# Optimization experiments

Measured on AMD Instinct MI355X. Metric: run time of the kernel, lower is better.

## Reference

```python
import jax, jax.numpy as jnp
import numpy as np


def setup_inputs() -> dict:
    key = jax.random.key(0)
    ks = jax.random.split(key, 8)
    bs, G, A, C, CM, D, H = 256, 169, 3, 5, 32, 1024, 512
    return {
        "boxes_sml0": jax.random.uniform(ks[0], (bs, G, A, C), dtype=jnp.float32),
        "masks_in0": jax.random.normal(ks[1], (bs, G, A, CM), dtype=jnp.float32),
        "feat": jax.random.normal(ks[2], (bs, D, 13, 13), dtype=jnp.float32),
        "lang_feat": jax.random.normal(ks[3], (bs, H), dtype=jnp.float32),
        "W_vs": jax.random.normal(ks[4], (D, H), dtype=jnp.float32) * 0.02,
        "b_vs": jnp.zeros((H,), dtype=jnp.float32),
        "W_ts": jax.random.normal(ks[5], (H, H), dtype=jnp.float32) * 0.02,
        "b_ts": jnp.zeros((H,), dtype=jnp.float32),
        "select_num": 32,
    }


def reference(boxes_sml0, masks_in0, feat, lang_feat, W_vs, b_vs, W_ts, b_ts, select_num):
    bs, G, A, C = boxes_sml0.shape
    CM = masks_in0.shape[-1]
    D = feat.shape[1]

    # mean over anchors of objectness channel 4 -> top-k grid selection
    mean_score = jnp.mean(boxes_sml0[..., 4], axis=2)           # [bs, G]
    _, idx = jax.lax.top_k(mean_score, select_num)              # [bs, k]

    # scatter-mask + masked_select in torch == gather of selected grids
    boxes_new = jnp.take_along_axis(boxes_sml0, idx[:, :, None, None], axis=1)  # [bs,k,A,C]
    masks_new = jnp.take_along_axis(masks_in0, idx[:, :, None, None], axis=1)   # [bs,k,A,CM]

    # gather visual features of selected grids, project
    i_all = feat.reshape(bs, D, -1).transpose(0, 2, 1)          # [bs, G, D]
    i_sel = jnp.take_along_axis(i_all, idx[:, :, None], axis=1) # [bs, k, D]
    x_new = i_sel @ W_vs + b_vs                                 # [bs, k, H]
    y_new = lang_feat @ W_ts + b_ts                             # [bs, H]

    # head: visual-text similarity, pick top grid per batch
    sim = jnp.einsum('bkh,bh->bk', x_new, y_new)                # [bs, k]
    maxval = jnp.max(sim, axis=1)                               # [bs]
    pred = jnp.argmax(sim, axis=1)                              # [bs]

    sel_b = jnp.take_along_axis(boxes_new, pred[:, None, None, None], axis=1)[:, 0]  # [bs,A,C]
    sel_m = jnp.take_along_axis(masks_new, pred[:, None, None, None], axis=1)[:, 0]  # [bs,A,CM]

    # cxcywh -> xyxy with original in-place overwrite semantics
    cx, cy, w, h = sel_b[..., 0], sel_b[..., 1], sel_b[..., 2], sel_b[..., 3]
    x1 = cx - w / 2
    y1 = cy - h / 2
    x2 = x1 + w
    y2 = y1 + h
    refined = jnp.concatenate(
        [jnp.stack([x1, y1, x2, y2], axis=-1), sel_b[..., 4:]], axis=-1)  # [bs,A,C]

    # pick anchor with max objectness, gather 5-dim box and mask coeffs
    aidx = jnp.argmax(refined[..., 4], axis=1)                  # [bs]
    box_new = jnp.take_along_axis(refined[..., :5], aidx[:, None, None], axis=1)  # [bs,1,5]
    mask_new = jnp.take_along_axis(sel_m, aidx[:, None, None], axis=1)            # [bs,1,CM]
    return box_new, mask_new, maxval
```

## Files before the change

### kernel.cpp

```cpp
#include <hip/hip_runtime.h>
#include <cfloat>
#include <cstdint>

#define GBM 64
#define GBN 64
#define GBK 64
#define GPAD 68

#define G_    169
#define D_    1024
#define SLAB  256
#define ROWG  8
#define NGRP  32
#define GRPF  1352
#define NV    338
#define SPL   8

typedef unsigned int u32;

__device__ __forceinline__ void gload_lds16(const float* g, float* l) {
    __builtin_amdgcn_global_load_lds(
        (const __attribute__((address_space(1))) u32*)g,
        (__attribute__((address_space(3))) u32*)l, 16, 0, 0);
}

__device__ __forceinline__ void stage_group(const float* gsrc, float* ldsbase, int lane) {
    #pragma unroll
    for (int j = 0; j < 6; j++) {
        int idx = j * 64 + lane;
        if (idx < NV)
            gload_lds16(gsrc + 4 * idx, ldsbase + j * 256);
    }
}

__global__ __launch_bounds__(256) void gemm_splitk(
    const float* __restrict__ A, const float* __restrict__ B,
    float* __restrict__ Cpart, int M, int N, int K)
{
    __shared__ __align__(16) float Asm[GBK][GPAD];
    __shared__ __align__(16) float Bsm[GBK][GPAD];
    int t  = threadIdx.x;
    int m0 = blockIdx.y * GBM, n0 = blockIdx.x * GBN;
    int ks = blockIdx.z * GBK;

    #pragma unroll
    for (int i = 0; i < 4; i++) {
        int v = t + 256 * i;
        int m = v >> 4, k4 = (v & 15) * 4;
        float4 x = *(const float4*)&A[(size_t)(m0 + m) * K + ks + k4];
        Asm[k4 + 0][m] = x.x; Asm[k4 + 1][m] = x.y;
        Asm[k4 + 2][m] = x.z; Asm[k4 + 3][m] = x.w;
    }
    #pragma unroll
    for (int i = 0; i < 4; i++) {
        int v = t + 256 * i;
        int r = v >> 4, c4 = (v & 15) * 4;
        *(float4*)&Bsm[r][c4] = *(const float4*)&B[(size_t)(ks + r) * N + n0 + c4];
    }
    __syncthreads();

    int r4 = (t >> 4) * 4, c4 = (t & 15) * 4;
    float acc[4][4] = {{0.f}};
    #pragma unroll
    for (int kk = 0; kk < GBK; kk++) {
        float4 a = *(const float4*)&Asm[kk][r4];
        float4 b = *(const float4*)&Bsm[kk][c4];
        float av[4] = {a.x, a.y, a.z, a.w};
        float bv[4] = {b.x, b.y, b.z, b.w};
        #pragma unroll
        for (int i = 0; i < 4; i++)
            #pragma unroll
            for (int j = 0; j < 4; j++) acc[i][j] += av[i] * bv[j];
    }
    float* Cp = Cpart + (size_t)blockIdx.z * M * N;
    #pragma unroll
    for (int i = 0; i < 4; i++) {
        float4 v = {acc[i][0], acc[i][1], acc[i][2], acc[i][3]};
        *(float4*)&Cp[(size_t)(m0 + r4 + i) * N + n0 + c4] = v;
    }
}

__global__ __launch_bounds__(256) void gemm2_fused(
    const float* __restrict__ py, const float* __restrict__ b_ts,
    const float* __restrict__ W, float* __restrict__ pz,
    int M, int N, int K)
{
    __shared__ __align__(16) float Asm[GBK][GPAD];
    __shared__ __align__(16) float Bsm[GBK][GPAD];
    int t  = threadIdx.x;
    int m0 = blockIdx.y * GBM, n0 = blockIdx.x * GBN;
    int ks = blockIdx.z * GBK;

    #pragma unroll
    for (int i = 0; i < 4; i++) {
        int v = t + 256 * i;
        int m = v >> 4, h4 = (v & 15) * 4;
        float4 x = *(const float4*)&b_ts[ks + h4];
        #pragma unroll
        for (int s = 0; s < SPL; s++) {
            float4 p = *(const float4*)&py[((size_t)s * M + m0 + m) * K + ks + h4];
            x.x += p.x; x.y += p.y; x.z += p.z; x.w += p.w;
        }
        Asm[h4 + 0][m] = x.x; Asm[h4 + 1][m] = x.y;
        Asm[h4 + 2][m] = x.z; Asm[h4 + 3][m] = x.w;
    }
    #pragma unroll
    for (int i = 0; i < 4; i++) {
        int v = t + 256 * i;
        int n = v >> 4, k4 = (v & 15) * 4;
        float4 x = *(const float4*)&W[(size_t)(n0 + n) * K + ks + k4];
        Bsm[k4 + 0][n] = x.x; Bsm[k4 + 1][n] = x.y;
        Bsm[k4 + 2][n] = x.z; Bsm[k4 + 3][n] = x.w;
    }
    __syncthreads();

    int r4 = (t >> 4) * 4, c4 = (t & 15) * 4;
    float acc[4][4] = {{0.f}};
    #pragma unroll
    for (int kk = 0; kk < GBK; kk++) {
        float4 a = *(const float4*)&Asm[kk][r4];
        float4 b = *(const float4*)&Bsm[kk][c4];
        float av[4] = {a.x, a.y, a.z, a.w};
        float bv[4] = {b.x, b.y, b.z, b.w};
        #pragma unroll
        for (int i = 0; i < 4; i++)
            #pragma unroll
            for (int j = 0; j < 4; j++) acc[i][j] += av[i] * bv[j];
    }
    float* Cp = pz + (size_t)blockIdx.z * M * N;
    #pragma unroll
    for (int i = 0; i < 4; i++) {
        float4 v = {acc[i][0], acc[i][1], acc[i][2], acc[i][3]};
        *(float4*)&Cp[(size_t)(m0 + r4 + i) * N + n0 + c4] = v;
    }
}

__global__ __launch_bounds__(256) void feat_final(
    const float* __restrict__ feat, const float* __restrict__ pz,
    const float* __restrict__ boxes, const float* __restrict__ masks,
    const float* __restrict__ py, const float* __restrict__ b_ts,
    const float* __restrict__ b_vs, const int* __restrict__ kptr,
    float* __restrict__ out_box, float* __restrict__ out_mask,
    float* __restrict__ out_max,
    int bs, int AN, int CH, int CM, int H)
{
    __shared__ __align__(16) float buf[4][2][GRPF];
    __shared__ __align__(16) float zs[D_];
    __shared__ float accw[4 * 192];
    __shared__ float simall[176];
    __shared__ float ms[176];
    __shared__ int   selg[176];
    __shared__ float simv[176];
    __shared__ float redw[4];
    __shared__ float bbs;
    __shared__ int   selp[2];

    const int b = blockIdx.x;
    const int t = threadIdx.x;
    const int w = t >> 6, lane = t & 63;

    {
        int h4 = t * 4;
        float4 s = {0.f, 0.f, 0.f, 0.f};
        #pragma unroll
        for (int sp = 0; sp < SPL; sp++) {
            float4 v = *(const float4*)&pz[((size_t)sp * bs + b) * D_ + h4];
            s.x += v.x; s.y += v.y; s.z += v.z; s.w += v.w;
        }
        *(float4*)&zs[h4] = s;
    }

    const float* gsrc = feat + ((size_t)b * D_ + (size_t)w * SLAB) * G_;
    stage_group(gsrc, buf[w][0], lane);

    float acc0 = 0.f, acc1 = 0.f, acc2 = 0.f;
    const bool g2 = lane < (G_ - 128);
    int cur = 0;
    for (int gi = 0; gi < NGRP; gi++) {
        if (gi + 1 < NGRP) {
            stage_group(gsrc + (size_t)(gi + 1) * GRPF, buf[w][cur ^ 1], lane);
            asm volatile("s_waitcnt vmcnt(6)" ::: "memory");
        } else {
            asm volatile("s_waitcnt vmcnt(0)" ::: "memory");
        }
        __builtin_amdgcn_sched_barrier(0);
        const float* bp = buf[w][cur];
        const float* zp = &zs[w * SLAB + gi * ROWG];
        #pragma unroll
        for (int r = 0; r < ROWG; r++) {
            float zv = zp[r];
            acc0 += bp[r * G_ + lane] * zv;
            acc1 += bp[r * G_ + lane + 64] * zv;
            if (g2) acc2 += bp[r * G_ + lane + 128] * zv;
        }
        cur ^= 1;
    }
    accw[w * 192 + lane]       = acc0;
    accw[w * 192 + lane + 64]  = acc1;
    if (g2) accw[w * 192 + lane + 128] = acc2;
    __syncthreads();

    int k = *kptr; if (k > G_) k = G_;

    if (t < G_) {
        simall[t] = accw[t] + accw[192 + t] + accw[384 + t] + accw[576 + t];
        const float* bp = boxes + (size_t)(b * G_ + t) * AN * CH;
        float s = 0.f;
        for (int a = 0; a < AN; a++) s += bp[a * CH + 4];
        ms[t] = s / (float)AN;
    }
    float part = 0.f;
    for (int h = t; h < H; h += 256) {
        float yv = b_ts[h];
        #pragma unroll
        for (int s = 0; s < SPL; s++) yv += py[((size_t)s * bs + b) * H + h];
        part += b_vs[h] * yv;
    }
    #pragma unroll
    for (int off = 32; off > 0; off >>= 1) part += __shfl_down(part, off);
    if ((t & 63) == 0) redw[t >> 6] = part;
    __syncthreads();
    if (t == 0) bbs = redw[0] + redw[1] + redw[2] + redw[3];

    if (t < G_) {
        float mv = ms[t];
        int rank = 0;
        for (int g = 0; g < G_; g++) {
            float o = ms[g];
            rank += (int)((o > mv) | ((o == mv) & (g < t)));
        }
        if (rank < k) selg[rank] = t;
    }
    __syncthreads();

    if (t < k) simv[t] = simall[selg[t]];
    __syncthreads();

    if (t == 0) {
        float best = -FLT_MAX; int br = 0;
        for (int r = 0; r < k; r++) if (simv[r] > best) { best = simv[r]; br = r; }
        int gs = selg[br];
        const float* bp = boxes + (size_t)(b * G_ + gs) * AN * CH;
        float bo = -FLT_MAX; int ai = 0;
        for (int a = 0; a < AN; a++) { float o = bp[a * CH + 4]; if (o > bo) { bo = o; ai = a; } }
        float cx = bp[ai * CH + 0], cy = bp[ai * CH + 1];
        float ww = bp[ai * CH + 2], hh = bp[ai * CH + 3];
        float x1 = cx - ww * 0.5f, y1 = cy - hh * 0.5f;
        out_box[(size_t)b * CH + 0] = x1;
        out_box[(size_t)b * CH + 1] = y1;
        out_box[(size_t)b * CH + 2] = x1 + ww;
        out_box[(size_t)b * CH + 3] = y1 + hh;
        for (int c = 4; c < CH; c++) out_box[(size_t)b * CH + c] = bp[ai * CH + c];
        out_max[b] = best + bbs;
        selp[0] = gs; selp[1] = ai;
    }
    __syncthreads();
    if (t < CM) {
        out_mask[(size_t)b * CM + t] =
            masks[((size_t)(b * G_ + selp[0]) * AN + selp[1]) * CM + t];
    }
}

extern "C" void kernel_launch(void* const* d_in, const int* in_sizes, int n_in,
                              void* d_out, int out_size, void* d_ws, size_t ws_size,
                              hipStream_t stream)
{
    const float* boxes = (const float*)d_in[0];
    const float* masks = (const float*)d_in[1];
    const float* feat  = (const float*)d_in[2];
    const float* lang  = (const float*)d_in[3];
    const float* W_vs  = (const float*)d_in[4];
    const float* b_vs  = (const float*)d_in[5];
    const float* W_ts  = (const float*)d_in[6];
    const float* b_ts  = (const float*)d_in[7];
    const int*   kptr  = (const int*)d_in[8];

    int H  = in_sizes[5];
    int D  = in_sizes[4] / H;
    int bs = in_sizes[3] / H;
    int AN = 3;
    int CH = in_sizes[0] / (bs * G_ * AN);
    int CM = in_sizes[1] / (bs * G_ * AN);

    float* py = (float*)d_ws;
    float* pz = py + (size_t)SPL * bs * H;

    float* out_box  = (float*)d_out;
    float* out_mask = out_box + (size_t)bs * CH;
    float* out_max  = out_mask + (size_t)bs * CM;

    dim3 g1(H / GBN, bs / GBM, SPL);
    gemm_splitk<<<g1, 256, 0, stream>>>(lang, W_ts, py, bs, H, H);
    dim3 g2(D / GBN, bs / GBM, SPL);
    gemm2_fused<<<g2, 256, 0, stream>>>(py, b_ts, W_vs, pz, bs, D, H);
    feat_final<<<bs, 256, 0, stream>>>(feat, pz, boxes, masks, py, b_ts, b_vs,
                                       kptr, out_box, out_mask, out_max,
                                       bs, AN, CH, CM, H);
}
```

Before: 60.99 us.

## Use 8 waves and triple-buffered LDS staging in feat_final

Doubles the block to 512 threads (8 waves, each handling a 128-channel slab) and moves from double to triple buffering of the feature staging, with two groups in flight and adjusted vmcnt waits. The aim is more memory-level parallelism per CU for the bandwidth-bound feat reduction over the 1024x169 per-batch slab. It also adds a missing __syncthreads after filling zs, which the wider slab layout now requires. LDS use grows to about 8*3*1352 floats (~130KB), which may limit occupancy to one block per CU or exceed the LDS budget.

```diff
diff --git a/kernel.cpp b/kernel.cpp
--- a/kernel.cpp
+++ b/kernel.cpp
@@ -9,11 +9,13 @@
 
 #define G_    169
 #define D_    1024
-#define SLAB  256
+#define NW    8
+#define SLAB  128
 #define ROWG  8
-#define NGRP  32
+#define NGRP  16
 #define GRPF  1352
 #define NV    338
+#define NBUF  3
 #define SPL   8
 
 typedef unsigned int u32;
@@ -135,7 +137,7 @@
     }
 }
 
-__global__ __launch_bounds__(256) void feat_final(
+__global__ __launch_bounds__(512) void feat_final(
     const float* __restrict__ feat, const float* __restrict__ pz,
     const float* __restrict__ boxes, const float* __restrict__ masks,
     const float* __restrict__ py, const float* __restrict__ b_ts,
@@ -144,14 +146,14 @@
     float* __restrict__ out_max,
     int bs, int AN, int CH, int CM, int H)
 {
-    __shared__ __align__(16) float buf[4][2][GRPF];
+    __shared__ __align__(16) float buf[NW][NBUF][GRPF];
     __shared__ __align__(16) float zs[D_];
-    __shared__ float accw[4 * 192];
+    __shared__ float accw[NW * 192];
     __shared__ float simall[176];
     __shared__ float ms[176];
     __shared__ int   selg[176];
     __shared__ float simv[176];
-    __shared__ float redw[4];
+    __shared__ float redw[NW];
     __shared__ float bbs;
     __shared__ int   selp[2];
 
@@ -160,31 +162,34 @@
     const int w = t >> 6, lane = t & 63;
 
     {
-        int h4 = t * 4;
-        float4 s = {0.f, 0.f, 0.f, 0.f};
+        int h2 = t * 2;
+        float2 s = {0.f, 0.f};
         #pragma unroll
         for (int sp = 0; sp < SPL; sp++) {
-            float4 v = *(const float4*)&pz[((size_t)sp * bs + b) * D_ + h4];
-            s.x += v.x; s.y += v.y; s.z += v.z; s.w += v.w;
-        }
-        *(float4*)&zs[h4] = s;
-    }
+            float2 v = *(const float2*)&pz[((size_t)sp * bs + b) * D_ + h2];
+            s.x += v.x; s.y += v.y;
+        }
+        *(float2*)&zs[h2] = s;
+    }
+    __syncthreads();
 
     const float* gsrc = feat + ((size_t)b * D_ + (size_t)w * SLAB) * G_;
-    stage_group(gsrc, buf[w][0], lane);
+    stage_group(gsrc,        buf[w][0], lane);
+    stage_group(gsrc + GRPF, buf[w][1], lane);
 
     float acc0 = 0.f, acc1 = 0.f, acc2 = 0.f;
     const bool g2 = lane < (G_ - 128);
-    int cur = 0;
     for (int gi = 0; gi < NGRP; gi++) {
-        if (gi + 1 < NGRP) {
-            stage_group(gsrc + (size_t)(gi + 1) * GRPF, buf[w][cur ^ 1], lane);
+        if (gi + 2 < NGRP) {
+            stage_group(gsrc + (size_t)(gi + 2) * GRPF, buf[w][(gi + 2) % NBUF], lane);
+            asm volatile("s_waitcnt vmcnt(12)" ::: "memory");
+        } else if (gi + 1 < NGRP) {
             asm volatile("s_waitcnt vmcnt(6)" ::: "memory");
         } else {
             asm volatile("s_waitcnt vmcnt(0)" ::: "memory");
         }
         __builtin_amdgcn_sched_barrier(0);
-        const float* bp = buf[w][cur];
+        const float* bp = buf[w][gi % NBUF];
         const float* zp = &zs[w * SLAB + gi * ROWG];
         #pragma unroll
         for (int r = 0; r < ROWG; r++) {
@@ -193,7 +198,6 @@
             acc1 += bp[r * G_ + lane + 64] * zv;
             if (g2) acc2 += bp[r * G_ + lane + 128] * zv;
         }
-        cur ^= 1;
     }
     accw[w * 192 + lane]       = acc0;
     accw[w * 192 + lane + 64]  = acc1;
@@ -203,24 +207,34 @@
     int k = *kptr; if (k > G_) k = G_;
 
     if (t < G_) {
-        simall[t] = accw[t] + accw[192 + t] + accw[384 + t] + accw[576 + t];
+        float s = 0.f;
+        #pragma unroll
+        for (int ww = 0; ww < NW; ww++) s += accw[ww * 192 + t];
+        simall[t] = s;
         const float* bp = boxes + (size_t)(b * G_ + t) * AN * CH;
+        float o = 0.f;
+        for (int a = 0; a < AN; a++) o += bp[a * CH + 4];
+        ms[t] = o / (float)AN;
+    }
+    {
+        float part = 0.f;
+        for (int h = t; h < H; h += 512) {
+            float yv = b_ts[h];
+            #pragma unroll
+            for (int s = 0; s < SPL; s++) yv += py[((size_t)s * bs + b) * H + h];
+            part += b_vs[h] * yv;
+        }
+        #pragma unroll
+        for (int off = 32; off > 0; off >>= 1) part += __shfl_down(part, off);
+        if (lane == 0) redw[w] = part;
+    }
+    __syncthreads();
+    if (t == 0) {
         float s = 0.f;
-        for (int a = 0; a < AN; a++) s += bp[a * CH + 4];
-        ms[t] = s / (float)AN;
-    }
-    float part = 0.f;
-    for (int h = t; h < H; h += 256) {
-        float yv = b_ts[h];
-        #pragma unroll
-        for (int s = 0; s < SPL; s++) yv += py[((size_t)s * bs + b) * H + h];
-        part += b_vs[h] * yv;
-    }
-    #pragma unroll
-    for (int off = 32; off > 0; off >>= 1) part += __shfl_down(part, off);
-    if ((t & 63) == 0) redw[t >> 6] = part;
-    __syncthreads();
-    if (t == 0) bbs = redw[0] + redw[1] + redw[2] + redw[3];
+        #pragma unroll
+        for (int ww = 0; ww < NW; ww++) s += redw[ww];
+        bbs = s;
+    }
 
     if (t < G_) {
         float mv = ms[t];
@@ -293,7 +307,7 @@
     gemm_splitk<<<g1, 256, 0, stream>>>(lang, W_ts, py, bs, H, H);
     dim3 g2(D / GBN, bs / GBM, SPL);
     gemm2_fused<<<g2, 256, 0, stream>>>(py, b_ts, W_vs, pz, bs, D, H);
-    feat_final<<<bs, 256, 0, stream>>>(feat, pz, boxes, masks, py, b_ts, b_vs,
+    feat_final<<<bs, 512, 0, stream>>>(feat, pz, boxes, masks, py, b_ts, b_vs,
                                        kptr, out_box, out_mask, out_max,
                                        bs, AN, CH, CM, H);
 }
```

Result: faster. 57.68 us (-5.4%).

## Split feature dot-product across D into separate kernel with triple-buffered LDS staging

Applied to the files above, without the earlier changes.

The per-batch feature-dot kernel is split into a feat_dot kernel launched over an (8 D-slices × bs) grid and a separate finalize kernel. Each feat_dot block reduces a 128-channel slice with a three-stage global-to-LDS prefetch, reads z values by wave shuffle instead of an LDS copy, and writes partial similarity scores to workspace. finalize sums the 8 partials only for the selected top-k grids. This raises the block count from 256 to 2048 to hide the latency of the 177 MB feat read, at the cost of an extra launch and a partial-sum round trip through workspace.

```diff
diff --git a/kernel.cpp b/kernel.cpp
--- a/kernel.cpp
+++ b/kernel.cpp
@@ -9,11 +9,12 @@
 
 #define G_    169
 #define D_    1024
-#define SLAB  256
-#define ROWG  8
-#define NGRP  32
-#define GRPF  1352
-#define NV    338
+#define DSPLIT 8
+#define ROWG  4
+#define NGRP  8
+#define CHF   676
+#define CNV   169
+#define NBUF  3
 #define SPL   8
 
 typedef unsigned int u32;
@@ -24,12 +25,12 @@
         (__attribute__((address_space(3))) u32*)l, 16, 0, 0);
 }
 
-__device__ __forceinline__ void stage_group(const float* gsrc, float* ldsbase, int lane) {
-    #pragma unroll
-    for (int j = 0; j < 6; j++) {
+__device__ __forceinline__ void stage4(const float* g, float* l, int lane) {
+    #pragma unroll
+    for (int j = 0; j < 3; j++) {
         int idx = j * 64 + lane;
-        if (idx < NV)
-            gload_lds16(gsrc + 4 * idx, ldsbase + j * 256);
+        if (idx < CNV)
+            gload_lds16(g + 4 * idx, l + j * 256);
     }
 }
 
@@ -135,75 +136,78 @@
     }
 }
 
-__global__ __launch_bounds__(256) void feat_final(
+__global__ __launch_bounds__(256) void feat_dot(
     const float* __restrict__ feat, const float* __restrict__ pz,
+    float* __restrict__ s_part, int bs)
+{
+    __shared__ __align__(16) float buf[4][NBUF][CHF];
+    __shared__ float accw[4 * 176];
+    const int b = blockIdx.y, ds = blockIdx.x;
+    const int t = threadIdx.x, w = t >> 6, lane = t & 63;
+
+    float zreg = 0.f;
+    {
+        int zi = ds * 128 + w * 32 + (lane & 31);
+        #pragma unroll
+        for (int s = 0; s < SPL; s++)
+            zreg += pz[((size_t)s * bs + b) * D_ + zi];
+    }
+
+    const float* gsrc = feat + ((size_t)b * D_ + ds * 128 + w * 32) * G_;
+    stage4(gsrc,       buf[w][0], lane);
+    stage4(gsrc + CHF, buf[w][1], lane);
+
+    float acc0 = 0.f, acc1 = 0.f, acc2 = 0.f;
+    const bool g2 = lane < (G_ - 128);
+    for (int gi = 0; gi < NGRP; gi++) {
+        if (gi + 2 < NGRP) {
+            stage4(gsrc + (size_t)(gi + 2) * CHF, buf[w][(gi + 2) % NBUF], lane);
+            asm volatile("s_waitcnt vmcnt(6)" ::: "memory");
+        } else if (gi + 1 < NGRP) {
+            asm volatile("s_waitcnt vmcnt(3)" ::: "memory");
+        } else {
+            asm volatile("s_waitcnt vmcnt(0)" ::: "memory");
+        }
+        __builtin_amdgcn_sched_barrier(0);
+        const float* bp = buf[w][gi % NBUF];
+        #pragma unroll
+        for (int r = 0; r < ROWG; r++) {
+            float zv = __shfl(zreg, gi * 4 + r, 64);
+            acc0 += bp[r * G_ + lane] * zv;
+            acc1 += bp[r * G_ + lane + 64] * zv;
+            if (g2) acc2 += bp[r * G_ + lane + 128] * zv;
+        }
+    }
+    accw[w * 176 + lane]      = acc0;
+    accw[w * 176 + lane + 64] = acc1;
+    if (g2) accw[w * 176 + lane + 128] = acc2;
+    __syncthreads();
+    if (t < G_) {
+        float s = accw[t] + accw[176 + t] + accw[352 + t] + accw[528 + t];
+        s_part[((size_t)b * G_ + t) * DSPLIT + ds] = s;
+    }
+}
+
+__global__ __launch_bounds__(256) void finalize(
     const float* __restrict__ boxes, const float* __restrict__ masks,
-    const float* __restrict__ py, const float* __restrict__ b_ts,
-    const float* __restrict__ b_vs, const int* __restrict__ kptr,
+    const float* __restrict__ s_part, const float* __restrict__ py,
+    const float* __restrict__ b_ts, const float* __restrict__ b_vs,
+    const int* __restrict__ kptr,
     float* __restrict__ out_box, float* __restrict__ out_mask,
     float* __restrict__ out_max,
-    int bs, int AN, int CH, int CM, int H)
-{
-    __shared__ __align__(16) float buf[4][2][GRPF];
-    __shared__ __align__(16) float zs[D_];
-    __shared__ float accw[4 * 192];
-    __shared__ float simall[176];
+    int AN, int CH, int CM, int H, int bs)
+{
     __shared__ float ms[176];
     __shared__ int   selg[176];
     __shared__ float simv[176];
     __shared__ float redw[4];
-    __shared__ float bbs;
-    __shared__ int   selp[2];
-
-    const int b = blockIdx.x;
-    const int t = threadIdx.x;
-    const int w = t >> 6, lane = t & 63;
-
-    {
-        int h4 = t * 4;
-        float4 s = {0.f, 0.f, 0.f, 0.f};
-        #pragma unroll
-        for (int sp = 0; sp < SPL; sp++) {
-            float4 v = *(const float4*)&pz[((size_t)sp * bs + b) * D_ + h4];
-            s.x += v.x; s.y += v.y; s.z += v.z; s.w += v.w;
-        }
-        *(float4*)&zs[h4] = s;
-    }
-
-    const float* gsrc = feat + ((size_t)b * D_ + (size_t)w * SLAB) * G_;
-    stage_group(gsrc, buf[w][0], lane);
-
-    float acc0 = 0.f, acc1 = 0.f, acc2 = 0.f;
-    const bool g2 = lane < (G_ - 128);
-    int cur = 0;
-    for (int gi = 0; gi < NGRP; gi++) {
-        if (gi + 1 < NGRP) {
-            stage_group(gsrc + (size_t)(gi + 1) * GRPF, buf[w][cur ^ 1], lane);
-            asm volatile("s_waitcnt vmcnt(6)" ::: "memory");
-        } else {
-            asm volatile("s_waitcnt vmcnt(0)" ::: "memory");
-        }
-        __builtin_amdgcn_sched_barrier(0);
-        const float* bp = buf[w][cur];
-        const float* zp = &zs[w * SLAB + gi * ROWG];
-        #pragma unroll
-        for (int r = 0; r < ROWG; r++) {
-            float zv = zp[r];
-            acc0 += bp[r * G_ + lane] * zv;
-            acc1 += bp[r * G_ + lane + 64] * zv;
-            if (g2) acc2 += bp[r * G_ + lane + 128] * zv;
-        }
-        cur ^= 1;
-    }
-    accw[w * 192 + lane]       = acc0;
-    accw[w * 192 + lane + 64]  = acc1;
-    if (g2) accw[w * 192 + lane + 128] = acc2;
-    __syncthreads();
-
+    __shared__ float bb_s;
+    __shared__ int   sel_pair[2];
+
+    int b = blockIdx.x, t = threadIdx.x;
     int k = *kptr; if (k > G_) k = G_;
 
     if (t < G_) {
-        simall[t] = accw[t] + accw[192 + t] + accw[384 + t] + accw[576 + t];
         const float* bp = boxes + (size_t)(b * G_ + t) * AN * CH;
         float s = 0.f;
         for (int a = 0; a < AN; a++) s += bp[a * CH + 4];
@@ -220,7 +224,7 @@
     for (int off = 32; off > 0; off >>= 1) part += __shfl_down(part, off);
     if ((t & 63) == 0) redw[t >> 6] = part;
     __syncthreads();
-    if (t == 0) bbs = redw[0] + redw[1] + redw[2] + redw[3];
+    if (t == 0) bb_s = redw[0] + redw[1] + redw[2] + redw[3];
 
     if (t < G_) {
         float mv = ms[t];
@@ -233,7 +237,13 @@
     }
     __syncthreads();
 
-    if (t < k) simv[t] = simall[selg[t]];
+    if (t < k) {
+        const float* sp = s_part + ((size_t)b * G_ + selg[t]) * DSPLIT;
+        float s = 0.f;
+        #pragma unroll
+        for (int i = 0; i < DSPLIT; i++) s += sp[i];
+        simv[t] = s;
+    }
     __syncthreads();
 
     if (t == 0) {
@@ -244,20 +254,20 @@
         float bo = -FLT_MAX; int ai = 0;
         for (int a = 0; a < AN; a++) { float o = bp[a * CH + 4]; if (o > bo) { bo = o; ai = a; } }
         float cx = bp[ai * CH + 0], cy = bp[ai * CH + 1];
-        float ww = bp[ai * CH + 2], hh = bp[ai * CH + 3];
-        float x1 = cx - ww * 0.5f, y1 = cy - hh * 0.5f;
+        float w  = bp[ai * CH + 2], hh = bp[ai * CH + 3];
+        float x1 = cx - w * 0.5f, y1 = cy - hh * 0.5f;
         out_box[(size_t)b * CH + 0] = x1;
         out_box[(size_t)b * CH + 1] = y1;
-        out_box[(size_t)b * CH + 2] = x1 + ww;
+        out_box[(size_t)b * CH + 2] = x1 + w;
         out_box[(size_t)b * CH + 3] = y1 + hh;
         for (int c = 4; c < CH; c++) out_box[(size_t)b * CH + c] = bp[ai * CH + c];
-        out_max[b] = best + bbs;
-        selp[0] = gs; selp[1] = ai;
+        out_max[b] = best + bb_s;
+        sel_pair[0] = gs; sel_pair[1] = ai;
     }
     __syncthreads();
     if (t < CM) {
         out_mask[(size_t)b * CM + t] =
-            masks[((size_t)(b * G_ + selp[0]) * AN + selp[1]) * CM + t];
+            masks[((size_t)(b * G_ + sel_pair[0]) * AN + sel_pair[1]) * CM + t];
     }
 }
 
@@ -282,8 +292,9 @@
     int CH = in_sizes[0] / (bs * G_ * AN);
     int CM = in_sizes[1] / (bs * G_ * AN);
 
-    float* py = (float*)d_ws;
-    float* pz = py + (size_t)SPL * bs * H;
+    float* py     = (float*)d_ws;
+    float* pz     = py + (size_t)SPL * bs * H;
+    float* s_part = pz + (size_t)SPL * bs * D;
 
     float* out_box  = (float*)d_out;
     float* out_mask = out_box + (size_t)bs * CH;
@@ -293,7 +304,9 @@
     gemm_splitk<<<g1, 256, 0, stream>>>(lang, W_ts, py, bs, H, H);
     dim3 g2(D / GBN, bs / GBM, SPL);
     gemm2_fused<<<g2, 256, 0, stream>>>(py, b_ts, W_vs, pz, bs, D, H);
-    feat_final<<<bs, 256, 0, stream>>>(feat, pz, boxes, masks, py, b_ts, b_vs,
-                                       kptr, out_box, out_mask, out_max,
-                                       bs, AN, CH, CM, H);
-}
+    dim3 gC(DSPLIT, bs);
+    feat_dot<<<gC, 256, 0, stream>>>(feat, pz, s_part, bs);
+    finalize<<<bs, 256, 0, stream>>>(boxes, masks, s_part, py, b_ts, b_vs, kptr,
+                                     out_box, out_mask, out_max,
+                                     AN, CH, CM, H, bs);
+}
```

New measurement: 60.88 us. Within noise of the previous version (-0.2%).
